# Performance work log

Hardware: AMD Instinct MI355X
Metric: run time of the kernel (lower is better)

Reference implementation:

```python
import jax, jax.numpy as jnp
import numpy as np

NF4_LEVELS = jnp.array([-1.0, -0.6962, -0.5251, -0.3949, -0.2844, -0.1848, -0.0911, 0.0,
                        0.0796, 0.1609, 0.2461, 0.3379, 0.4407, 0.5626, 0.723, 1.0], dtype=jnp.float32)
OUT_FEATURES = 4096
IN_FEATURES = 4096
BLOCK_SIZE = 1024
NUM_BLOCKS = OUT_FEATURES * IN_FEATURES // BLOCK_SIZE  # 16384

def setup_inputs() -> dict:
    key = jax.random.key(0)
    k1, k2, k3 = jax.random.split(key, 3)
    x = jax.random.normal(k1, (4, 2048, IN_FEATURES), dtype=jnp.float32)
    quant_indices = jax.random.randint(k2, (NUM_BLOCKS, BLOCK_SIZE), 0, 16, dtype=jnp.int32)
    scales = jax.random.uniform(k3, (NUM_BLOCKS,), dtype=jnp.float32)
    return {"x": x, "quant_indices": quant_indices, "scales": scales}

def reference(x, quant_indices, scales):
    # Block-wise NF4 dequantization: levels lookup * per-block absmax scale
    deq = NF4_LEVELS[quant_indices] * scales[:, None]          # [num_blocks, block_size]
    W = deq.reshape(OUT_FEATURES, IN_FEATURES)                 # [out, in]
    # F.linear(x, W): y = x @ W.T
    return jnp.einsum('bsi,oi->bso', x, W)
```

## Files before the change

kernel.cpp:

```cpp
#include <hip/hip_runtime.h>

typedef unsigned short u16;
typedef __attribute__((ext_vector_type(4))) float  f32x4;
typedef __attribute__((ext_vector_type(4))) int    i32x4;
typedef __attribute__((ext_vector_type(4))) unsigned u32x4;
typedef __attribute__((ext_vector_type(8))) short  shortx8;

__device__ __constant__ float NF4C[16] = {
    -1.0f, -0.6962f, -0.5251f, -0.3949f, -0.2844f, -0.1848f, -0.0911f, 0.0f,
     0.0796f, 0.1609f, 0.2461f, 0.3379f, 0.4407f, 0.5626f, 0.723f, 1.0f};

__device__ __forceinline__ unsigned f2bf(float f) {
    unsigned u = __float_as_uint(f);
    return (u + 0x7FFFu + ((u >> 16) & 1u)) >> 16;
}

__device__ __forceinline__ void ld_lds16(const u16* g, u16* l) {
    __builtin_amdgcn_global_load_lds(
        (const __attribute__((address_space(1))) void*)g,
        (__attribute__((address_space(3))) void*)l,
        16, 0, 0);
}


__global__ __launch_bounds__(256) void cvt_x(const float* __restrict__ x,
                                             u16* __restrict__ xb) {
    const size_t i = ((size_t)blockIdx.x * 256 + threadIdx.x) * 8;
    f32x4 f0 = __builtin_nontemporal_load((const f32x4*)(x + i));
    f32x4 f1 = __builtin_nontemporal_load((const f32x4*)(x + i + 4));
    u32x4 o;
    o[0] = f2bf(f0[0]) | (f2bf(f0[1]) << 16);
    o[1] = f2bf(f0[2]) | (f2bf(f0[3]) << 16);
    o[2] = f2bf(f1[0]) | (f2bf(f1[1]) << 16);
    o[3] = f2bf(f1[2]) | (f2bf(f1[3]) << 16);
    *(u32x4*)(xb + i) = o;
}

__global__ __launch_bounds__(256) void deq_w(const int* __restrict__ qi,
                                             const float* __restrict__ sc,
                                             u16* __restrict__ wb) {
    const size_t i = ((size_t)blockIdx.x * 256 + threadIdx.x) * 8;
    const float s = sc[i >> 10];
    i32x4 q0 = __builtin_nontemporal_load((const i32x4*)(qi + i));
    i32x4 q1 = __builtin_nontemporal_load((const i32x4*)(qi + i + 4));
    u32x4 o;
    o[0] = f2bf(NF4C[q0[0]] * s) | (f2bf(NF4C[q0[1]] * s) << 16);
    o[1] = f2bf(NF4C[q0[2]] * s) | (f2bf(NF4C[q0[3]] * s) << 16);
    o[2] = f2bf(NF4C[q1[0]] * s) | (f2bf(NF4C[q1[1]] * s) << 16);
    o[3] = f2bf(NF4C[q1[2]] * s) | (f2bf(NF4C[q1[3]] * s) << 16);
    *(u32x4*)(wb + i) = o;
}


#define BM 256
#define BN 256
#define BK 64

template<int MODE>
__device__ __forceinline__ void kgroup(
    const u16* __restrict__ Ar, const u16* __restrict__ Br,
    u16* dA1, u16* dB1,
    u16* dBc,
    const u16* gA1, const u16* gB1,
    int wm, int wn, int r16, int c0, int c1,
    f32x4 (&acc)[8][4])
{
    constexpr size_t K = 4096;
    shortx8 a[4], b[4];

#pragma unroll
    for (int j = 0; j < 4; j++)
        b[j] = *(const shortx8*)&Br[(wn + j * 16 + r16) * 64 + c0 * 8];
#pragma unroll
    for (int i = 0; i < 4; i++)
        a[i] = *(const shortx8*)&Ar[(wm + i * 16 + r16) * 64 + c0 * 8];
    if constexpr (MODE <= 1) {
        ld_lds16(gB1 + 128 * K, dB1 + 128 * 64);
        ld_lds16(gB1 + 192 * K, dB1 + 192 * 64);
    }
    asm volatile("s_barrier" ::: "memory");
    asm volatile("s_waitcnt lgkmcnt(0)" ::: "memory");
    __builtin_amdgcn_s_setprio(1);
#pragma unroll
    for (int i = 0; i < 4; i++)
#pragma unroll
        for (int j = 0; j < 4; j++)
            acc[i][j] = __builtin_amdgcn_mfma_f32_16x16x32_bf16(a[i], b[j], acc[i][j], 0, 0, 0);
    __builtin_amdgcn_s_setprio(0);
    if constexpr (MODE <= 1) asm volatile("s_waitcnt vmcnt(4)" ::: "memory");
    asm volatile("s_barrier" ::: "memory");

#pragma unroll
    for (int i = 0; i < 4; i++)
        a[i] = *(const shortx8*)&Ar[(wm + 64 + i * 16 + r16) * 64 + c0 * 8];
    if constexpr (MODE <= 1) {
        ld_lds16(gA1,           dA1);
        ld_lds16(gA1 + 128 * K, dA1 + 128 * 64);
    }
    asm volatile("s_barrier" ::: "memory");
    asm volatile("s_waitcnt lgkmcnt(0)" ::: "memory");
    __builtin_amdgcn_s_setprio(1);
#pragma unroll
    for (int i = 0; i < 4; i++)
#pragma unroll
        for (int j = 0; j < 4; j++)
            acc[4 + i][j] = __builtin_amdgcn_mfma_f32_16x16x32_bf16(a[i], b[j], acc[4 + i][j], 0, 0, 0);
    __builtin_amdgcn_s_setprio(0);
    asm volatile("s_barrier" ::: "memory");

#pragma unroll
    for (int j = 0; j < 4; j++)
        b[j] = *(const shortx8*)&Br[(wn + j * 16 + r16) * 64 + c1 * 8];
#pragma unroll
    for (int i = 0; i < 4; i++)
        a[i] = *(const shortx8*)&Ar[(wm + i * 16 + r16) * 64 + c1 * 8];
    if constexpr (MODE <= 1) {
        ld_lds16(gA1 +  64 * K, dA1 +  64 * 64);
        ld_lds16(gA1 + 192 * K, dA1 + 192 * 64);
    }
    asm volatile("s_barrier" ::: "memory");
    asm volatile("s_waitcnt lgkmcnt(0)" ::: "memory");
    __builtin_amdgcn_s_setprio(1);
#pragma unroll
    for (int i = 0; i < 4; i++)
#pragma unroll
        for (int j = 0; j < 4; j++)
            acc[i][j] = __builtin_amdgcn_mfma_f32_16x16x32_bf16(a[i], b[j], acc[i][j], 0, 0, 0);
    __builtin_amdgcn_s_setprio(0);
    asm volatile("s_barrier" ::: "memory");

#pragma unroll
    for (int i = 0; i < 4; i++)
        a[i] = *(const shortx8*)&Ar[(wm + 64 + i * 16 + r16) * 64 + c1 * 8];
    if constexpr (MODE == 0) {
        ld_lds16(gB1 + 64,           dBc);
        ld_lds16(gB1 + 64 + 64 * K,  dBc + 64 * 64);
    }
    asm volatile("s_barrier" ::: "memory");
    asm volatile("s_waitcnt lgkmcnt(0)" ::: "memory");
    __builtin_amdgcn_s_setprio(1);
#pragma unroll
    for (int i = 0; i < 4; i++)
#pragma unroll
        for (int j = 0; j < 4; j++)
            acc[4 + i][j] = __builtin_amdgcn_mfma_f32_16x16x32_bf16(a[i], b[j], acc[4 + i][j], 0, 0, 0);
    __builtin_amdgcn_s_setprio(0);
    if constexpr (MODE == 0)      asm volatile("s_waitcnt vmcnt(4)" ::: "memory");
    else if constexpr (MODE == 1) asm volatile("s_waitcnt vmcnt(0)" ::: "memory");
    asm volatile("s_barrier" ::: "memory");
}

__global__ __launch_bounds__(512, 2) void gemm_bt(const u16* __restrict__ A,
                                                  const u16* __restrict__ B,
                                                  float* __restrict__ C) {
    constexpr size_t K = 4096;
    constexpr int N = 4096;
    __shared__ __align__(16) u16 As[2][BM * BK];
    __shared__ __align__(16) u16 Bs[2][BN * BK];

    const int t    = threadIdx.x;
    const int wave = t >> 6;
    const int lane = t & 63;
    const int quad = lane >> 4;
    const int r16  = lane & 15;

    const int id  = blockIdx.x;
    const int xcd = id & 7;
    const int loc = id >> 3;
    const int bm  = (xcd * 4 + (loc >> 4)) * BM;
    const int bn  = (loc & 15) * BN;

    const int lrow = (wave << 3) + (lane >> 3);
    const int lch  = (lane & 7) ^ (lane >> 3);
    const u16* sA = A + (size_t)(bm + lrow) * K + lch * 8;
    const u16* sB = B + (size_t)(bn + lrow) * K + lch * 8;

    const int w512 = wave * 512;
    u16* dA0 = &As[0][w512];  u16* dA1 = &As[1][w512];
    u16* dB0 = &Bs[0][w512];  u16* dB1 = &Bs[1][w512];

    const int wm = (wave >> 2) * 128;
    const int wn = (wave & 3) * 64;
    const int c0 = quad ^ (r16 & 7);
    const int c1 = c0 ^ 4;

    f32x4 acc[8][4];
#pragma unroll
    for (int i = 0; i < 8; i++)
#pragma unroll
        for (int j = 0; j < 4; j++) acc[i][j] = (f32x4)0.0f;

#pragma unroll
    for (int r0 = 0; r0 < 256; r0 += 64) {
        ld_lds16(sA + (size_t)r0 * K, dA0 + r0 * 64);
        ld_lds16(sB + (size_t)r0 * K, dB0 + r0 * 64);
    }
    ld_lds16(sB + 64,                 dB1);
    ld_lds16(sB + 64 + (size_t)64 * K, dB1 + 64 * 64);
    asm volatile("s_waitcnt vmcnt(2)" ::: "memory");
    asm volatile("s_barrier" ::: "memory");

    const u16* gA1 = sA + 64;
    const u16* gB1 = sB + 64;
#pragma unroll 1
    for (int u = 0; u < 62; u += 2) {
        kgroup<0>(As[0], Bs[0], dA1, dB1, dB0, gA1, gB1, wm, wn, r16, c0, c1, acc);
        gA1 += 64; gB1 += 64;
        kgroup<0>(As[1], Bs[1], dA0, dB0, dB1, gA1, gB1, wm, wn, r16, c0, c1, acc);
        gA1 += 64; gB1 += 64;
    }
    kgroup<1>(As[0], Bs[0], dA1, dB1, dB0, gA1, gB1, wm, wn, r16, c0, c1, acc);
    kgroup<2>(As[1], Bs[1], dA0, dB0, dB1, gA1, gB1, wm, wn, r16, c0, c1, acc);

#pragma unroll
    for (int i = 0; i < 8; i++) {
        const int row0 = bm + wm + i * 16 + quad * 4;
#pragma unroll
        for (int j = 0; j < 4; j++) {
            const int col = bn + wn + j * 16 + r16;
            float* cp = &C[(size_t)row0 * N + col];
#pragma unroll
            for (int v = 0; v < 4; ++v)
                cp[(size_t)v * N] = acc[i][j][v];
        }
    }
}


__global__ __launch_bounds__(256) void fallback_gemm(const float* __restrict__ x,
                                                     const int* __restrict__ qi,
                                                     const float* __restrict__ sc,
                                                     float* __restrict__ y) {
    __shared__ float xs[16][16];
    __shared__ float wsm[16][17];
    const int tx = threadIdx.x, ty = threadIdx.y;
    const int m = blockIdx.y * 16 + ty;
    const int nrow = blockIdx.x * 16 + ty;
    float acc = 0.f;
    for (int k0 = 0; k0 < 4096; k0 += 16) {
        xs[ty][tx] = x[(size_t)m * 4096 + k0 + tx];
        const size_t fi = (size_t)nrow * 4096 + k0 + tx;
        wsm[ty][tx] = NF4C[qi[fi]] * sc[fi >> 10];
        __syncthreads();
#pragma unroll
        for (int kk = 0; kk < 16; kk++) acc += xs[ty][kk] * wsm[tx][kk];
        __syncthreads();
    }
    y[(size_t)m * 4096 + blockIdx.x * 16 + tx] = acc;
}


extern "C" void kernel_launch(void* const* d_in, const int* in_sizes, int n_in,
                              void* d_out, int out_size, void* d_ws, size_t ws_size,
                              hipStream_t stream) {
    const float* x  = (const float*)d_in[0];
    const int*   qi = (const int*)d_in[1];
    const float* sc = (const float*)d_in[2];
    float* y = (float*)d_out;

    const int M = 8192, N = 4096, K = 4096;
    const size_t xb_bytes = (size_t)M * K * 2;
    const size_t wb_bytes = (size_t)N * K * 2;

    if (ws_size >= xb_bytes + wb_bytes) {
        u16* xb = (u16*)d_ws;
        u16* wb = (u16*)((char*)d_ws + xb_bytes);
        cvt_x<<<(M * K) / (256 * 8), 256, 0, stream>>>(x, xb);
        deq_w<<<(N * K) / (256 * 8), 256, 0, stream>>>(qi, sc, wb);
        gemm_bt<<<(M / BM) * (N / BN), 512, 0, stream>>>(xb, wb, y);
    } else {
        dim3 block(16, 16);
        dim3 grid(N / 16, M / 16);
        fallback_gemm<<<grid, block, 0, stream>>>(x, qi, sc, y);
    }
}
```

Before: 491.8 us.

## Merge prep kernels and drop most per-phase barriers in GEMM k-loop

Merges the x conversion and weight dequant kernels into one grid-stride prep kernel, saving a launch. In the GEMM inner group, removes most s_barrier and lgkmcnt waits between phases and keeps a separate a2 register set so LDS reads and MFMAs interleave more freely. Only one barrier per half-group plus a vmcnt wait remain. This risks LDS read-after-write races between the async global-to-LDS loads and other waves' reads, and raises register pressure.

Measured after the change: 478.3 us. 2.7% less time.

```diff
diff --git a/kernel.cpp b/kernel.cpp
--- a/kernel.cpp
+++ b/kernel.cpp
@@ -23,32 +23,37 @@
 }
 
 
-__global__ __launch_bounds__(256) void cvt_x(const float* __restrict__ x,
-                                             u16* __restrict__ xb) {
-    const size_t i = ((size_t)blockIdx.x * 256 + threadIdx.x) * 8;
-    f32x4 f0 = __builtin_nontemporal_load((const f32x4*)(x + i));
-    f32x4 f1 = __builtin_nontemporal_load((const f32x4*)(x + i + 4));
-    u32x4 o;
-    o[0] = f2bf(f0[0]) | (f2bf(f0[1]) << 16);
-    o[1] = f2bf(f0[2]) | (f2bf(f0[3]) << 16);
-    o[2] = f2bf(f1[0]) | (f2bf(f1[1]) << 16);
-    o[3] = f2bf(f1[2]) | (f2bf(f1[3]) << 16);
-    *(u32x4*)(xb + i) = o;
-}
-
-__global__ __launch_bounds__(256) void deq_w(const int* __restrict__ qi,
-                                             const float* __restrict__ sc,
-                                             u16* __restrict__ wb) {
-    const size_t i = ((size_t)blockIdx.x * 256 + threadIdx.x) * 8;
-    const float s = sc[i >> 10];
-    i32x4 q0 = __builtin_nontemporal_load((const i32x4*)(qi + i));
-    i32x4 q1 = __builtin_nontemporal_load((const i32x4*)(qi + i + 4));
-    u32x4 o;
-    o[0] = f2bf(NF4C[q0[0]] * s) | (f2bf(NF4C[q0[1]] * s) << 16);
-    o[1] = f2bf(NF4C[q0[2]] * s) | (f2bf(NF4C[q0[3]] * s) << 16);
-    o[2] = f2bf(NF4C[q1[0]] * s) | (f2bf(NF4C[q1[1]] * s) << 16);
-    o[3] = f2bf(NF4C[q1[2]] * s) | (f2bf(NF4C[q1[3]] * s) << 16);
-    *(u32x4*)(wb + i) = o;
+__global__ __launch_bounds__(256) void prep(const float* __restrict__ x,
+                                            const int* __restrict__ qi,
+                                            const float* __restrict__ sc,
+                                            u16* __restrict__ xb,
+                                            u16* __restrict__ wb) {
+    const size_t nthr = (size_t)gridDim.x * 256;
+    const size_t tid  = (size_t)blockIdx.x * 256 + threadIdx.x;
+
+    for (size_t c = tid; c < (33554432u / 8); c += nthr) {
+        const size_t i = c * 8;
+        f32x4 f0 = __builtin_nontemporal_load((const f32x4*)(x + i));
+        f32x4 f1 = __builtin_nontemporal_load((const f32x4*)(x + i + 4));
+        u32x4 o;
+        o[0] = f2bf(f0[0]) | (f2bf(f0[1]) << 16);
+        o[1] = f2bf(f0[2]) | (f2bf(f0[3]) << 16);
+        o[2] = f2bf(f1[0]) | (f2bf(f1[1]) << 16);
+        o[3] = f2bf(f1[2]) | (f2bf(f1[3]) << 16);
+        *(u32x4*)(xb + i) = o;
+    }
+    for (size_t c = tid; c < (16777216u / 8); c += nthr) {
+        const size_t i = c * 8;
+        const float s = sc[i >> 10];
+        i32x4 q0 = __builtin_nontemporal_load((const i32x4*)(qi + i));
+        i32x4 q1 = __builtin_nontemporal_load((const i32x4*)(qi + i + 4));
+        u32x4 o;
+        o[0] = f2bf(NF4C[q0[0]] * s) | (f2bf(NF4C[q0[1]] * s) << 16);
+        o[1] = f2bf(NF4C[q0[2]] * s) | (f2bf(NF4C[q0[3]] * s) << 16);
+        o[2] = f2bf(NF4C[q1[0]] * s) | (f2bf(NF4C[q1[1]] * s) << 16);
+        o[3] = f2bf(NF4C[q1[2]] * s) | (f2bf(NF4C[q1[3]] * s) << 16);
+        *(u32x4*)(wb + i) = o;
+    }
 }
 
 
@@ -66,7 +71,7 @@
     f32x4 (&acc)[8][4])
 {
     constexpr size_t K = 4096;
-    shortx8 a[4], b[4];
+    shortx8 a[4], a2[4], b[4];
 
 #pragma unroll
     for (int j = 0; j < 4; j++)
@@ -78,8 +83,6 @@
         ld_lds16(gB1 + 128 * K, dB1 + 128 * 64);
         ld_lds16(gB1 + 192 * K, dB1 + 192 * 64);
     }
-    asm volatile("s_barrier" ::: "memory");
-    asm volatile("s_waitcnt lgkmcnt(0)" ::: "memory");
     __builtin_amdgcn_s_setprio(1);
 #pragma unroll
     for (int i = 0; i < 4; i++)
@@ -87,26 +90,21 @@
         for (int j = 0; j < 4; j++)
             acc[i][j] = __builtin_amdgcn_mfma_f32_16x16x32_bf16(a[i], b[j], acc[i][j], 0, 0, 0);
     __builtin_amdgcn_s_setprio(0);
-    if constexpr (MODE <= 1) asm volatile("s_waitcnt vmcnt(4)" ::: "memory");
-    asm volatile("s_barrier" ::: "memory");
-
-#pragma unroll
-    for (int i = 0; i < 4; i++)
-        a[i] = *(const shortx8*)&Ar[(wm + 64 + i * 16 + r16) * 64 + c0 * 8];
+
+#pragma unroll
+    for (int i = 0; i < 4; i++)
+        a2[i] = *(const shortx8*)&Ar[(wm + 64 + i * 16 + r16) * 64 + c0 * 8];
     if constexpr (MODE <= 1) {
         ld_lds16(gA1,           dA1);
         ld_lds16(gA1 + 128 * K, dA1 + 128 * 64);
     }
-    asm volatile("s_barrier" ::: "memory");
-    asm volatile("s_waitcnt lgkmcnt(0)" ::: "memory");
-    __builtin_amdgcn_s_setprio(1);
-#pragma unroll
-    for (int i = 0; i < 4; i++)
-#pragma unroll
-        for (int j = 0; j < 4; j++)
-            acc[4 + i][j] = __builtin_amdgcn_mfma_f32_16x16x32_bf16(a[i], b[j], acc[4 + i][j], 0, 0, 0);
-    __builtin_amdgcn_s_setprio(0);
-    asm volatile("s_barrier" ::: "memory");
+    __builtin_amdgcn_s_setprio(1);
+#pragma unroll
+    for (int i = 0; i < 4; i++)
+#pragma unroll
+        for (int j = 0; j < 4; j++)
+            acc[4 + i][j] = __builtin_amdgcn_mfma_f32_16x16x32_bf16(a2[i], b[j], acc[4 + i][j], 0, 0, 0);
+    __builtin_amdgcn_s_setprio(0);
 
 #pragma unroll
     for (int j = 0; j < 4; j++)
@@ -118,8 +116,6 @@
         ld_lds16(gA1 +  64 * K, dA1 +  64 * 64);
         ld_lds16(gA1 + 192 * K, dA1 + 192 * 64);
     }
-    asm volatile("s_barrier" ::: "memory");
-    asm volatile("s_waitcnt lgkmcnt(0)" ::: "memory");
     __builtin_amdgcn_s_setprio(1);
 #pragma unroll
     for (int i = 0; i < 4; i++)
@@ -127,27 +123,30 @@
         for (int j = 0; j < 4; j++)
             acc[i][j] = __builtin_amdgcn_mfma_f32_16x16x32_bf16(a[i], b[j], acc[i][j], 0, 0, 0);
     __builtin_amdgcn_s_setprio(0);
-    asm volatile("s_barrier" ::: "memory");
-
-#pragma unroll
-    for (int i = 0; i < 4; i++)
-        a[i] = *(const shortx8*)&Ar[(wm + 64 + i * 16 + r16) * 64 + c1 * 8];
+    if constexpr (MODE == 0)
+        asm volatile("s_barrier" ::: "memory");
+
+#pragma unroll
+    for (int i = 0; i < 4; i++)
+        a2[i] = *(const shortx8*)&Ar[(wm + 64 + i * 16 + r16) * 64 + c1 * 8];
     if constexpr (MODE == 0) {
-        ld_lds16(gB1 + 64,           dBc);
-        ld_lds16(gB1 + 64 + 64 * K,  dBc + 64 * 64);
-    }
-    asm volatile("s_barrier" ::: "memory");
-    asm volatile("s_waitcnt lgkmcnt(0)" ::: "memory");
-    __builtin_amdgcn_s_setprio(1);
-#pragma unroll
-    for (int i = 0; i < 4; i++)
-#pragma unroll
-        for (int j = 0; j < 4; j++)
-            acc[4 + i][j] = __builtin_amdgcn_mfma_f32_16x16x32_bf16(a[i], b[j], acc[4 + i][j], 0, 0, 0);
-    __builtin_amdgcn_s_setprio(0);
-    if constexpr (MODE == 0)      asm volatile("s_waitcnt vmcnt(4)" ::: "memory");
-    else if constexpr (MODE == 1) asm volatile("s_waitcnt vmcnt(0)" ::: "memory");
-    asm volatile("s_barrier" ::: "memory");
+        ld_lds16(gB1 + 64,          dBc);
+        ld_lds16(gB1 + 64 + 64 * K, dBc + 64 * 64);
+    }
+    __builtin_amdgcn_s_setprio(1);
+#pragma unroll
+    for (int i = 0; i < 4; i++)
+#pragma unroll
+        for (int j = 0; j < 4; j++)
+            acc[4 + i][j] = __builtin_amdgcn_mfma_f32_16x16x32_bf16(a2[i], b[j], acc[4 + i][j], 0, 0, 0);
+    __builtin_amdgcn_s_setprio(0);
+    if constexpr (MODE == 0) {
+        asm volatile("s_waitcnt vmcnt(2)" ::: "memory");
+        asm volatile("s_barrier" ::: "memory");
+    } else if constexpr (MODE == 1) {
+        asm volatile("s_waitcnt vmcnt(0)" ::: "memory");
+        asm volatile("s_barrier" ::: "memory");
+    }
 }
 
 __global__ __launch_bounds__(512, 2) void gemm_bt(const u16* __restrict__ A,
@@ -195,7 +194,7 @@
         ld_lds16(sA + (size_t)r0 * K, dA0 + r0 * 64);
         ld_lds16(sB + (size_t)r0 * K, dB0 + r0 * 64);
     }
-    ld_lds16(sB + 64,                 dB1);
+    ld_lds16(sB + 64,                  dB1);
     ld_lds16(sB + 64 + (size_t)64 * K, dB1 + 64 * 64);
     asm volatile("s_waitcnt vmcnt(2)" ::: "memory");
     asm volatile("s_barrier" ::: "memory");
@@ -265,8 +264,7 @@
     if (ws_size >= xb_bytes + wb_bytes) {
         u16* xb = (u16*)d_ws;
         u16* wb = (u16*)((char*)d_ws + xb_bytes);
-        cvt_x<<<(M * K) / (256 * 8), 256, 0, stream>>>(x, xb);
-        deq_w<<<(N * K) / (256 * 8), 256, 0, stream>>>(qi, sc, wb);
+        prep<<<2048, 256, 0, stream>>>(x, qi, sc, xb, wb);
         gemm_bt<<<(M / BM) * (N / BN), 512, 0, stream>>>(xb, wb, y);
     } else {
         dim3 block(16, 16);
```
